# Kernel optimization log

Measured on AMD Instinct MI355X. Metric: run time of the kernel, lower is better.

## Reference

```python
import jax, jax.numpy as jnp
import numpy as np

B, T, C = 2, 2048, 1024
H, G, D = 16, 4, 64            # n_head, n_group (KV heads), d_head
GROUP = H // G                 # query heads per KV head
WIN, SINK = 512, 4             # sliding window, attention sink
BASE = 10000.0
SCALE = D ** -0.5


def _rope(x, pos):
    """Interleaved RoPE on per-head dim. x: [B, T, h, D]."""
    t = x.shape[1]
    inv_freq = 1.0 / (BASE ** (jnp.arange(0, D, 2, dtype=jnp.float32) / D))  # [D/2]
    theta = (pos + jnp.arange(t, dtype=jnp.float32))[:, None] * inv_freq[None, :]  # [T, D/2]
    cos = jnp.cos(theta)[None, :, None, :]  # [1,T,1,D/2]
    sin = jnp.sin(theta)[None, :, None, :]
    xe, xo = x[..., 0::2], x[..., 1::2]
    re = xe * cos - xo * sin
    ro = xe * sin + xo * cos
    return jnp.stack([re, ro], axis=-1).reshape(x.shape)


def setup_inputs() -> dict:
    key = jax.random.key(0)
    ks = jax.random.split(key, 9)
    s = 0.02
    return {
        "x":  jax.random.normal(ks[0], (B, T, C), jnp.float32),
        "Wq": jax.random.normal(ks[1], (C, H * D), jnp.float32) * s,
        "bq": jnp.zeros((H * D,), jnp.float32),
        "Wk": jax.random.normal(ks[2], (C, G * D), jnp.float32) * s,
        "bk": jnp.zeros((G * D,), jnp.float32),
        "Wv": jax.random.normal(ks[3], (C, G * D), jnp.float32) * s,
        "bv": jnp.zeros((G * D,), jnp.float32),
        "Wo": jax.random.normal(ks[4], (C, C), jnp.float32) * s,
        "bo": jnp.zeros((C,), jnp.float32),
        "pos": 0,
    }


def reference(x, Wq, bq, Wk, bk, Wv, bv, Wo, bo, pos):
    b, t, c = x.shape
    q = (x @ Wq + bq).reshape(b, t, H, D)   # [B,T,H,D]
    k = (x @ Wk + bk).reshape(b, t, G, D)   # [B,T,G,D]
    v = (x @ Wv + bv).reshape(b, t, G, D)
    q = _rope(q, pos)
    k = _rope(k, pos)
    q = q.transpose(0, 2, 1, 3)             # [B,H,T,D]
    k = k.transpose(0, 2, 1, 3)             # [B,G,T,D]
    v = v.transpose(0, 2, 1, 3)
    # GQA: repeat-interleave KV heads to match query heads
    k = jnp.repeat(k, GROUP, axis=1)        # [B,H,T,D]
    v = jnp.repeat(v, GROUP, axis=1)
    # sliding-window + sink causal mask
    i = jnp.arange(t)[:, None]
    j = jnp.arange(t)[None, :]
    mask = (i >= j) & ((j >= i - WIN) | (j < SINK))  # [T,T] bool
    scores = jnp.einsum("bhqd,bhkd->bhqk", q, k) * SCALE
    neg = jnp.finfo(scores.dtype).min
    scores = jnp.where(mask[None, None], scores, neg)
    attn = jax.nn.softmax(scores, axis=-1)
    out = jnp.einsum("bhqk,bhkd->bhqd", attn, v)  # [B,H,T,D]
    out = out.transpose(0, 2, 1, 3).reshape(b, t, c)
    return out @ Wo + bo
```

## Files before the change

### kernel.cpp

```cpp
#include <hip/hip_runtime.h>
#include <stdint.h>
#include <math.h>

typedef short v8s __attribute__((ext_vector_type(8)));
typedef float v4f __attribute__((ext_vector_type(4)));

#define DEVI static __device__ __forceinline__
#define AS1 __attribute__((address_space(1)))
#define AS3 __attribute__((address_space(3)))

static constexpr int Bn = 2;
static constexpr int Tn = 2048;
static constexpr int Hn = 16;
static constexpr int Gn = 4;
static constexpr int NQKV = 1536;
static constexpr int WIN = 512;
static constexpr int SINKN = 4;
#define SCALE_L2E (0.125f * 1.4426950408889634f)

DEVI unsigned short f2bf(float f) {
  unsigned u = __float_as_uint(f);
  u += 0x7fffu + ((u >> 16) & 1u);
  return (unsigned short)(u >> 16);
}
DEVI float bf2f(unsigned short h) { return __uint_as_float(((unsigned)h) << 16); }
DEVI unsigned pack_bf2(float hi, float lo) {
  return __builtin_amdgcn_perm(__float_as_uint(hi), __float_as_uint(lo), 0x07060302u);
}

__global__ __launch_bounds__(256) void k_transpose_all(const float* __restrict__ Wq,
                                                       const float* __restrict__ Wk,
                                                       const float* __restrict__ Wv,
                                                       const float* __restrict__ Wo,
                                                       unsigned short* __restrict__ wt_qkv,
                                                       unsigned short* __restrict__ wt_o,
                                                       const int* __restrict__ posp,
                                                       float2* __restrict__ table,
                                                       const float* __restrict__ bq,
                                                       const float* __restrict__ bk,
                                                       const float* __restrict__ bv,
                                                       float* __restrict__ biasout,
                                                       const float* __restrict__ x,
                                                       unsigned short* __restrict__ xb) {
  int z = blockIdx.z;
  int tx = threadIdx.x, ty = threadIdx.y;
  if (z == 5) {
    int base = (blockIdx.y * 32 + blockIdx.x) * 256 + ty * 32 + tx;
    #pragma unroll
    for (int j = 0; j < 4; ++j) {
      int i = base + j * 262144;
      float4 v = ((const float4*)x)[i];
      ushort4 o;
      o.x = f2bf(v.x); o.y = f2bf(v.y); o.z = f2bf(v.z); o.w = f2bf(v.w);
      ((ushort4*)xb)[i] = o;
    }
    return;
  }
  if (z == 4) {
    int i = (blockIdx.y * 32 + blockIdx.x) * 256 + ty * 32 + tx;
    if (i < Tn * 32) {
      int t = i >> 5, d2 = i & 31;
      float inv = powf(10000.f, -(float)d2 / 32.f);
      float theta = (float)(posp[0] + t) * inv;
      float s, c;
      sincosf(theta, &s, &c);
      table[i] = make_float2(c, s);
    }
    if (i < NQKV)
      biasout[i] = (i < 1024) ? bq[i] * SCALE_L2E : (i < 1280 ? bk[i - 1024] : bv[i - 1280]);
    return;
  }
  const float* W; unsigned short* Wt; int N; float scale = 1.f;
  if (z == 0)      { W = Wq; Wt = wt_qkv;                 N = 1024; scale = SCALE_L2E; }
  else if (z == 1) { W = Wk; Wt = wt_qkv + 1024 * 1024;   N = 256; }
  else if (z == 2) { W = Wv; Wt = wt_qkv + 1280 * 1024;   N = 256; }
  else             { W = Wo; Wt = wt_o;                   N = 1024; }
  int n0 = blockIdx.x * 32, k0 = blockIdx.y * 32;
  if (n0 >= N) return;
  __shared__ float tile[32][33];
  #pragma unroll
  for (int yy = 0; yy < 4; ++yy)
    tile[ty + yy * 8][tx] = W[(size_t)(k0 + ty + yy * 8) * N + n0 + tx];
  __syncthreads();
  #pragma unroll
  for (int yy = 0; yy < 4; ++yy)
    Wt[(size_t)(n0 + ty + yy * 8) * 1024 + k0 + tx] = f2bf(tile[tx][ty + yy * 8] * scale);
}

template <bool F32OUT>
__global__ __launch_bounds__(256) void k_gemm_bt(const unsigned short* __restrict__ A,
                                                 const unsigned short* __restrict__ Bt,
                                                 const float* __restrict__ bias,
                                                 const float2* __restrict__ table,
                                                 float* __restrict__ outF,
                                                 unsigned short* __restrict__ outH,
                                                 unsigned short* __restrict__ vtH,
                                                 int M, int N, int K) {
  __shared__ char As[8192];
  __shared__ char Bs[16384];
  int nx = gridDim.x;
  int nwg = nx * gridDim.y;
  int id = blockIdx.y * nx + blockIdx.x;
  int swz = (id & 7) * (nwg >> 3) + (id >> 3);
  int m0 = (swz / nx) * 64, n0 = (swz % nx) * 128;

  int t = threadIdx.x, lane = t & 63, wave = t >> 6;
  int wm = wave >> 1, wn = wave & 1;
  int l15 = lane & 15, l4 = lane >> 4;
  v4f acc[2][4] = {};

  for (int k0 = 0; k0 < K; k0 += 64) {
    __syncthreads();
    #pragma unroll
    for (int p = 0; p < 2; ++p) {
      int cid = p * 256 + t;
      int row = cid >> 3, cc = cid & 7;
      const unsigned short* ga = A + (size_t)(m0 + row) * K + k0 + cc * 8;
      __builtin_amdgcn_global_load_lds((const AS1 void*)ga,
                                       (AS3 void*)(As + p * 4096 + wave * 1024), 16, 0, 0);
    }
    #pragma unroll
    for (int p = 0; p < 4; ++p) {
      int cid = p * 256 + t;
      int row = cid >> 3, cc = cid & 7;
      const unsigned short* gb = Bt + (size_t)(n0 + row) * K + k0 + cc * 8;
      __builtin_amdgcn_global_load_lds((const AS1 void*)gb,
                                       (AS3 void*)(Bs + p * 4096 + wave * 1024), 16, 0, 0);
    }
    __syncthreads();
    #pragma unroll
    for (int kk = 0; kk < 2; ++kk) {
      v8s af[2], bfr[4];
      #pragma unroll
      for (int mi = 0; mi < 2; ++mi)
        af[mi] = *(const v8s*)(As + (wm * 32 + mi * 16 + l15) * 128 + kk * 64 + l4 * 16);
      #pragma unroll
      for (int ni = 0; ni < 4; ++ni)
        bfr[ni] = *(const v8s*)(Bs + (wn * 64 + ni * 16 + l15) * 128 + kk * 64 + l4 * 16);
      #pragma unroll
      for (int mi = 0; mi < 2; ++mi)
        #pragma unroll
        for (int ni = 0; ni < 4; ++ni)
          acc[mi][ni] = __builtin_amdgcn_mfma_f32_16x16x32_bf16(af[mi], bfr[ni], acc[mi][ni], 0, 0, 0);
    }
  }

  if (!F32OUT && n0 >= 1280) {
    #pragma unroll
    for (int mi = 0; mi < 2; ++mi) {
      #pragma unroll
      for (int ni = 0; ni < 4; ++ni) {
        int col = n0 + wn * 64 + ni * 16 + l15;
        float bv = bias[col];
        int c2 = col - 1280;
        int gg = c2 >> 6, dd = c2 & 63;
        int row = m0 + wm * 32 + mi * 16 + l4 * 4;
        int bb = row >> 11, tt = row & 2047;
        ushort4 ov;
        ov.x = f2bf(acc[mi][ni][0] + bv);
        ov.y = f2bf(acc[mi][ni][1] + bv);
        ov.z = f2bf(acc[mi][ni][2] + bv);
        ov.w = f2bf(acc[mi][ni][3] + bv);
        *(ushort4*)(vtH + ((size_t)((bb * Gn + gg) * 64 + dd)) * Tn + tt) = ov;
      }
    }
  } else if (!F32OUT) {
    #pragma unroll
    for (int mi = 0; mi < 2; ++mi) {
      #pragma unroll
      for (int ni = 0; ni < 4; ++ni) {
        int col = n0 + wn * 64 + ni * 16 + l15;
        float bv = bias[col];
        int d2 = (col & 63) >> 1;
        bool even = !(col & 1);
        #pragma unroll
        for (int r = 0; r < 4; ++r) {
          int row = m0 + wm * 32 + mi * 16 + l4 * 4 + r;
          int tt = row & 2047;
          float2 cs = table[tt * 32 + d2];
          float v = acc[mi][ni][r] + bv;
          float prt = __shfl_xor(v, 1);
          float ov = even ? (v * cs.x - prt * cs.y) : (prt * cs.y + v * cs.x);
          outH[(size_t)row * N + col] = f2bf(ov);
        }
      }
    }
  } else {
    #pragma unroll
    for (int mi = 0; mi < 2; ++mi) {
      #pragma unroll
      for (int ni = 0; ni < 4; ++ni) {
        int col = n0 + wn * 64 + ni * 16 + l15;
        float bv = bias[col];
        #pragma unroll
        for (int r = 0; r < 4; ++r) {
          int row = m0 + wm * 32 + mi * 16 + l4 * 4 + r;
          outF[(size_t)row * N + col] = acc[mi][ni][r] + bv;
        }
      }
    }
  }
}

__global__ __launch_bounds__(512) void k_attn(const unsigned short* __restrict__ qkv,
                                              const unsigned short* __restrict__ vt,
                                              unsigned short* __restrict__ o) {
  __shared__ char smem[2 * 16384];
  int id = blockIdx.x;
  int half = id >> 8, r5 = id & 255;
  int h = r5 >> 4;
  int qtile = half ? (15 - (r5 & 15)) : (r5 & 15);
  int b = half;
  int qt0 = qtile * 128;
  int g = h >> 2;
  int t = threadIdx.x, lane = t & 63, wave = t >> 6;
  int l15 = lane & 15, l4 = lane >> 4;
  int qw0 = qt0 + wave * 16;

  int jt_end = (qt0 + 127) >> 6;
  int wstart = (qt0 > WIN) ? ((qt0 - WIN) >> 6) : 0;
  int nIt = (wstart > 0) ? (jt_end - wstart + 2) : (jt_end + 1);

  int sr = t >> 3, sc = t & 7;
  int scs = (sc ^ (sr & 7)) << 3;
  const unsigned short* gkb = qkv + (size_t)(b * Tn + sr) * NQKV + 1024 + g * 64 + scs;
  const unsigned short* gvb = vt + ((size_t)((b * Gn + g) * 64 + sr)) * Tn + scs;

  auto stageKV = [&](int buf, int j0) {
    __builtin_amdgcn_global_load_lds((const AS1 void*)(gkb + (size_t)j0 * NQKV),
                                     (AS3 void*)(smem + buf * 16384 + wave * 1024), 16, 0, 0);
    __builtin_amdgcn_global_load_lds((const AS1 void*)(gvb + j0),
                                     (AS3 void*)(smem + buf * 16384 + 8192 + wave * 1024), 16, 0, 0);
  };

  auto jt_of = [&](int it) { return (wstart > 0) ? (it == 0 ? 0 : wstart + it - 1) : it; };

  stageKV(0, jt_of(0) << 6);

  v8s Qf[2];
  #pragma unroll
  for (int hf = 0; hf < 2; ++hf)
    Qf[hf] = *(const v8s*)(qkv + (size_t)(b * Tn + qw0 + l15) * NQKV + h * 64 + hf * 32 + l4 * 8);

  float m = -INFINITY, lsm = 0.f;
  v4f accO[4] = {};

  __syncthreads();

  for (int it = 0; it < nIt; ++it) {
    int cur = it & 1;
    if (it + 1 < nIt) stageKV(cur ^ 1, jt_of(it + 1) << 6);
    int j0 = jt_of(it) << 6;

    bool skip = (j0 > qw0 + 15) || ((j0 + 63 < qw0 - WIN) && (j0 >= SINKN));
    if (!skip) {
      const char* Kb = smem + cur * 16384;
      const char* Vb = Kb + 8192;
      v4f s[4];
      #pragma unroll
      for (int kb = 0; kb < 4; ++kb) {
        int r = kb * 16 + l15;
        v8s kf0 = *(const v8s*)(Kb + r * 128 + ((l4 ^ (r & 7)) << 4));
        v8s kf1 = *(const v8s*)(Kb + r * 128 + (((4 + l4) ^ (r & 7)) << 4));
        v4f z = {};
        z = __builtin_amdgcn_mfma_f32_16x16x32_bf16(kf0, Qf[0], z, 0, 0, 0);
        s[kb] = __builtin_amdgcn_mfma_f32_16x16x32_bf16(kf1, Qf[1], z, 0, 0, 0);
      }
      bool needMask = !((j0 + 63 <= qw0) && (j0 >= qw0 + 15 - WIN));
      if (needMask) {
        #pragma unroll
        for (int kb = 0; kb < 4; ++kb)
          #pragma unroll
          for (int r = 0; r < 4; ++r) {
            int j = j0 + kb * 16 + l4 * 4 + r;
            int qg = qw0 + l15;
            bool valid = (j <= qg) && ((j >= qg - WIN) || (j < SINKN));
            s[kb][r] = valid ? s[kb][r] : -1e30f;
          }
      }
      float mt = -1e30f;
      #pragma unroll
      for (int kb = 0; kb < 4; ++kb)
        #pragma unroll
        for (int r = 0; r < 4; ++r) mt = fmaxf(mt, s[kb][r]);
      mt = fmaxf(mt, __shfl_xor(mt, 16));
      mt = fmaxf(mt, __shfl_xor(mt, 32));
      if (!__all(mt <= m + 8.f)) {
        float mnew = fmaxf(m, mt);
        float alpha = exp2f(m - mnew);
        lsm *= alpha;
        #pragma unroll
        for (int db = 0; db < 4; ++db) {
          accO[db][0] *= alpha; accO[db][1] *= alpha;
          accO[db][2] *= alpha; accO[db][3] *= alpha;
        }
        m = mnew;
      }
      float lsum = 0.f;
      unsigned pk[4][2];
      #pragma unroll
      for (int kb = 0; kb < 4; ++kb) {
        float p0 = exp2f(s[kb][0] - m);
        float p1 = exp2f(s[kb][1] - m);
        float p2 = exp2f(s[kb][2] - m);
        float p3 = exp2f(s[kb][3] - m);
        lsum += (p0 + p1) + (p2 + p3);
        pk[kb][0] = pack_bf2(p1, p0);
        pk[kb][1] = pack_bf2(p3, p2);
      }
      lsum += __shfl_xor(lsum, 16);
      lsum += __shfl_xor(lsum, 32);
      lsm += lsum;

      int src0 = ((2 * (l4 & 1)) << 4) | l15;
      int src1 = src0 + 16;
      bool hiSel = (l4 >> 1) & 1;
      #pragma unroll
      for (int kc = 0; kc < 2; ++kc) {
        int A0 = __shfl((int)pk[kc * 2][0], src0);
        int A1 = __shfl((int)pk[kc * 2][1], src0);
        int A2 = __shfl((int)pk[kc * 2][0], src1);
        int A3 = __shfl((int)pk[kc * 2][1], src1);
        int B0 = __shfl((int)pk[kc * 2 + 1][0], src0);
        int B1 = __shfl((int)pk[kc * 2 + 1][1], src0);
        int B2 = __shfl((int)pk[kc * 2 + 1][0], src1);
        int B3 = __shfl((int)pk[kc * 2 + 1][1], src1);
        union { int i[4]; v8s v; } u;
        u.i[0] = hiSel ? B0 : A0;
        u.i[1] = hiSel ? B1 : A1;
        u.i[2] = hiSel ? B2 : A2;
        u.i[3] = hiSel ? B3 : A3;
        #pragma unroll
        for (int db = 0; db < 4; ++db) {
          int d = db * 16 + l15;
          v8s vf = *(const v8s*)(Vb + d * 128 + (((kc * 4 + l4) ^ (d & 7)) << 4));
          accO[db] = __builtin_amdgcn_mfma_f32_16x16x32_bf16(vf, u.v, accO[db], 0, 0, 0);
        }
      }
    }
    __syncthreads();
  }

  float inv = 1.f / lsm;
  size_t orow = (size_t)(b * Tn + qw0 + l15) * 1024 + h * 64;
  #pragma unroll
  for (int db = 0; db < 4; ++db) {
    int d0 = db * 16 + l4 * 4;
    ushort4 ov;
    ov.x = f2bf(accO[db][0] * inv);
    ov.y = f2bf(accO[db][1] * inv);
    ov.z = f2bf(accO[db][2] * inv);
    ov.w = f2bf(accO[db][3] * inv);
    *(ushort4*)(o + orow + d0) = ov;
  }
}

extern "C" void kernel_launch(void* const* d_in, const int* in_sizes, int n_in,
                              void* d_out, int out_size, void* d_ws, size_t ws_size,
                              hipStream_t stream) {
  const float* x  = (const float*)d_in[0];
  const float* Wq = (const float*)d_in[1];
  const float* bq = (const float*)d_in[2];
  const float* Wk = (const float*)d_in[3];
  const float* bk = (const float*)d_in[4];
  const float* Wv = (const float*)d_in[5];
  const float* bv = (const float*)d_in[6];
  const float* Wo = (const float*)d_in[7];
  const float* bo = (const float*)d_in[8];
  const int*   pos = (const int*)d_in[9];
  float* out = (float*)d_out;

  char* ws = (char*)d_ws;
  unsigned short* xb      = (unsigned short*)(ws);
  unsigned short* wt_qkv  = (unsigned short*)(ws + 8388608);
  unsigned short* wt_o    = (unsigned short*)(ws + 11534336);
  float*          bias_q  = (float*)(ws + 13631488);
  float2*         table   = (float2*)(ws + 13637632);
  unsigned short* qkvb    = (unsigned short*)(ws + 14161920);
  unsigned short* vt      = (unsigned short*)(ws + 26744832);
  unsigned short* attno   = xb;

  k_transpose_all<<<dim3(32, 32, 6), dim3(32, 8), 0, stream>>>(Wq, Wk, Wv, Wo, wt_qkv, wt_o,
                                                               pos, table, bq, bk, bv, bias_q,
                                                               x, xb);
  k_gemm_bt<false><<<dim3(12, 64), 256, 0, stream>>>(xb, wt_qkv, bias_q, table, nullptr, qkvb, vt,
                                                     4096, NQKV, 1024);
  k_attn<<<512, 512, 0, stream>>>(qkvb, vt, attno);
  k_gemm_bt<true><<<dim3(8, 64), 256, 0, stream>>>(attno, wt_o, bo, nullptr, out, nullptr, nullptr,
                                                   4096, 1024, 1024);
}
```

Measured before the change: 90.33 us.

## Swizzle GEMM LDS tiles and route attention P through per-wave LDS

The GEMM kernel now XOR-swizzles the 16-byte column chunk by row when staging A and B into LDS, and reads fragments with the matching swizzle to avoid LDS bank conflicts. The attention kernel drops the cross-lane shuffle transpose of the bf16 probability tile. Each wave now writes P into a private, swizzled 2 KB LDS region and reads it back as an MFMA operand. It also adds s_setprio around the MFMA blocks. This trades many shuffles and selects for extra LDS traffic and a waitcnt, and raises LDS use per block to 48 KB, which could limit occupancy.

```diff
diff --git a/kernel.cpp b/kernel.cpp
--- a/kernel.cpp
+++ b/kernel.cpp
@@ -107,6 +107,7 @@
   int t = threadIdx.x, lane = t & 63, wave = t >> 6;
   int wm = wave >> 1, wn = wave & 1;
   int l15 = lane & 15, l4 = lane >> 4;
+  int l7 = l15 & 7;
   v4f acc[2][4] = {};
 
   for (int k0 = 0; k0 < K; k0 += 64) {
@@ -115,7 +116,7 @@
     for (int p = 0; p < 2; ++p) {
       int cid = p * 256 + t;
       int row = cid >> 3, cc = cid & 7;
-      const unsigned short* ga = A + (size_t)(m0 + row) * K + k0 + cc * 8;
+      const unsigned short* ga = A + (size_t)(m0 + row) * K + k0 + (cc ^ (row & 7)) * 8;
       __builtin_amdgcn_global_load_lds((const AS1 void*)ga,
                                        (AS3 void*)(As + p * 4096 + wave * 1024), 16, 0, 0);
     }
@@ -123,7 +124,7 @@
     for (int p = 0; p < 4; ++p) {
       int cid = p * 256 + t;
       int row = cid >> 3, cc = cid & 7;
-      const unsigned short* gb = Bt + (size_t)(n0 + row) * K + k0 + cc * 8;
+      const unsigned short* gb = Bt + (size_t)(n0 + row) * K + k0 + (cc ^ (row & 7)) * 8;
       __builtin_amdgcn_global_load_lds((const AS1 void*)gb,
                                        (AS3 void*)(Bs + p * 4096 + wave * 1024), 16, 0, 0);
     }
@@ -133,10 +134,10 @@
       v8s af[2], bfr[4];
       #pragma unroll
       for (int mi = 0; mi < 2; ++mi)
-        af[mi] = *(const v8s*)(As + (wm * 32 + mi * 16 + l15) * 128 + kk * 64 + l4 * 16);
+        af[mi] = *(const v8s*)(As + (wm * 32 + mi * 16 + l15) * 128 + (((kk * 4 + l4) ^ l7) << 4));
       #pragma unroll
       for (int ni = 0; ni < 4; ++ni)
-        bfr[ni] = *(const v8s*)(Bs + (wn * 64 + ni * 16 + l15) * 128 + kk * 64 + l4 * 16);
+        bfr[ni] = *(const v8s*)(Bs + (wn * 64 + ni * 16 + l15) * 128 + (((kk * 4 + l4) ^ l7) << 4));
       #pragma unroll
       for (int mi = 0; mi < 2; ++mi)
         #pragma unroll
@@ -205,7 +206,7 @@
 __global__ __launch_bounds__(512) void k_attn(const unsigned short* __restrict__ qkv,
                                               const unsigned short* __restrict__ vt,
                                               unsigned short* __restrict__ o) {
-  __shared__ char smem[2 * 16384];
+  __shared__ char smem[2 * 16384 + 16384];
   int id = blockIdx.x;
   int half = id >> 8, r5 = id & 255;
   int h = r5 >> 4;
@@ -215,7 +216,9 @@
   int g = h >> 2;
   int t = threadIdx.x, lane = t & 63, wave = t >> 6;
   int l15 = lane & 15, l4 = lane >> 4;
+  int l7 = l15 & 7;
   int qw0 = qt0 + wave * 16;
+  char* Pb = smem + 32768 + wave * 2048;
 
   int jt_end = (qt0 + 127) >> 6;
   int wstart = (qt0 > WIN) ? ((qt0 - WIN) >> 6) : 0;
@@ -257,6 +260,7 @@
       const char* Kb = smem + cur * 16384;
       const char* Vb = Kb + 8192;
       v4f s[4];
+      __builtin_amdgcn_s_setprio(1);
       #pragma unroll
       for (int kb = 0; kb < 4; ++kb) {
         int r = kb * 16 + l15;
@@ -266,6 +270,7 @@
         z = __builtin_amdgcn_mfma_f32_16x16x32_bf16(kf0, Qf[0], z, 0, 0, 0);
         s[kb] = __builtin_amdgcn_mfma_f32_16x16x32_bf16(kf1, Qf[1], z, 0, 0, 0);
       }
+      __builtin_amdgcn_s_setprio(0);
       bool needMask = !((j0 + 63 <= qw0) && (j0 >= qw0 + 15 - WIN));
       if (needMask) {
         #pragma unroll
@@ -297,7 +302,6 @@
         m = mnew;
       }
       float lsum = 0.f;
-      unsigned pk[4][2];
       #pragma unroll
       for (int kb = 0; kb < 4; ++kb) {
         float p0 = exp2f(s[kb][0] - m);
@@ -305,38 +309,29 @@
         float p2 = exp2f(s[kb][2] - m);
         float p3 = exp2f(s[kb][3] - m);
         lsum += (p0 + p1) + (p2 + p3);
-        pk[kb][0] = pack_bf2(p1, p0);
-        pk[kb][1] = pack_bf2(p3, p2);
+        unsigned lo = pack_bf2(p1, p0);
+        unsigned hi = pack_bf2(p3, p2);
+        unsigned long long w = ((unsigned long long)hi << 32) | lo;
+        *(unsigned long long*)(Pb + l15 * 128 + ((kb * 32 + l4 * 8) ^ (l7 << 4))) = w;
       }
       lsum += __shfl_xor(lsum, 16);
       lsum += __shfl_xor(lsum, 32);
       lsm += lsum;
-
-      int src0 = ((2 * (l4 & 1)) << 4) | l15;
-      int src1 = src0 + 16;
-      bool hiSel = (l4 >> 1) & 1;
+      asm volatile("s_waitcnt lgkmcnt(0)" ::: "memory");
+      __builtin_amdgcn_sched_barrier(0);
+
+      __builtin_amdgcn_s_setprio(1);
       #pragma unroll
       for (int kc = 0; kc < 2; ++kc) {
-        int A0 = __shfl((int)pk[kc * 2][0], src0);
-        int A1 = __shfl((int)pk[kc * 2][1], src0);
-        int A2 = __shfl((int)pk[kc * 2][0], src1);
-        int A3 = __shfl((int)pk[kc * 2][1], src1);
-        int B0 = __shfl((int)pk[kc * 2 + 1][0], src0);
-        int B1 = __shfl((int)pk[kc * 2 + 1][1], src0);
-        int B2 = __shfl((int)pk[kc * 2 + 1][0], src1);
-        int B3 = __shfl((int)pk[kc * 2 + 1][1], src1);
-        union { int i[4]; v8s v; } u;
-        u.i[0] = hiSel ? B0 : A0;
-        u.i[1] = hiSel ? B1 : A1;
-        u.i[2] = hiSel ? B2 : A2;
-        u.i[3] = hiSel ? B3 : A3;
+        v8s pfrag = *(const v8s*)(Pb + l15 * 128 + ((kc * 64 + l4 * 16) ^ (l7 << 4)));
         #pragma unroll
         for (int db = 0; db < 4; ++db) {
           int d = db * 16 + l15;
           v8s vf = *(const v8s*)(Vb + d * 128 + (((kc * 4 + l4) ^ (d & 7)) << 4));
-          accO[db] = __builtin_amdgcn_mfma_f32_16x16x32_bf16(vf, u.v, accO[db], 0, 0, 0);
+          accO[db] = __builtin_amdgcn_mfma_f32_16x16x32_bf16(vf, pfrag, accO[db], 0, 0, 0);
         }
       }
+      __builtin_amdgcn_s_setprio(0);
     }
     __syncthreads();
   }
```

Result: faster. 77.42 us (-14.3%).
